# Optimization experiments

Hardware: AMD Instinct MI355X
Metric: run time of the kernel (lower is better)

Reference implementation:

```python
import jax, jax.numpy as jnp
import numpy as np

PAD = 0

def setup_inputs() -> dict:
    key = jax.random.key(0)
    ks = jax.random.split(key, 16)
    B, S, D, F = 64, 512, 768, 256
    VOCAB = 32000
    # variable-length tweets: length in [8, S], rest is padding (token id PAD=0)
    lengths = jax.random.randint(ks[0], (B,), 8, S + 1)
    tok = jax.random.randint(ks[1], (B, S), 1, VOCAB)
    x = jnp.where(jnp.arange(S)[None, :] < lengths[:, None], tok, PAD)
    h = jax.random.normal(ks[2], (B, S, D), dtype=jnp.float32)
    sc = 0.02
    w2 = jax.random.normal(ks[3], (F, D, 2), dtype=jnp.float32) * sc
    b2 = jax.random.normal(ks[4], (F,), dtype=jnp.float32) * sc
    w3 = jax.random.normal(ks[5], (F, D, 3), dtype=jnp.float32) * sc
    b3 = jax.random.normal(ks[6], (F,), dtype=jnp.float32) * sc
    w4 = jax.random.normal(ks[7], (F, D, 4), dtype=jnp.float32) * sc
    b4 = jax.random.normal(ks[8], (F,), dtype=jnp.float32) * sc
    w5 = jax.random.normal(ks[9], (F, D, 5), dtype=jnp.float32) * sc
    b5 = jax.random.normal(ks[10], (F,), dtype=jnp.float32) * sc
    fc_w = jax.random.normal(ks[11], (1, 4 * F), dtype=jnp.float32) * sc
    fc_b = jax.random.normal(ks[12], (1,), dtype=jnp.float32) * sc
    return {"x": x, "h": h, "w2": w2, "b2": b2, "w3": w3, "b3": b3,
            "w4": w4, "b4": b4, "w5": w5, "b5": b5, "fc_w": fc_w, "fc_b": fc_b}


def _branch(hc, L, w, b):
    # hc: [B, D, S] front-compacted hidden states; w: [F, D, k]
    k = w.shape[-1]
    out = jax.lax.conv_general_dilated(
        hc, w, window_strides=(1,), padding='VALID',
        dimension_numbers=('NCH', 'OIH', 'NCH')) + b[None, :, None]  # [B,F,S-k+1]
    T = out.shape[-1]
    # conv position t is valid iff t + k - 1 < L  <=>  t < L - k + 1
    valid = jnp.arange(T)[None, :] < (L - k + 1)[:, None]           # [B,T]
    neg = jnp.asarray(-jnp.inf, out.dtype)
    pooled = jnp.max(jnp.where(valid[:, None, :], out, neg), axis=-1)  # [B,F]
    return jax.nn.relu(pooled)


def reference(x, h, w2, b2, w3, b3, w4, b4, w5, b5, fc_w, fc_b):
    mask = x != PAD                                   # [B,S]
    L = mask.sum(axis=1)                              # [B]
    # stable compaction: move non-pad token hidden states to the front, order preserved
    order = jnp.argsort(jnp.logical_not(mask), axis=1, stable=True)   # [B,S]
    hc = jnp.take_along_axis(h, order[..., None], axis=1)             # [B,S,D]
    hc = hc.transpose(0, 2, 1)                                        # [B,D,S]
    feats = jnp.concatenate([
        _branch(hc, L, w2, b2),
        _branch(hc, L, w3, b3),
        _branch(hc, L, w4, b4),
        _branch(hc, L, w5, b5),
    ], axis=-1)                                       # [B, 4F]
    logits = feats @ fc_w.T + fc_b                    # [B,1]
    return jax.nn.sigmoid(logits).squeeze(-1)         # [B]
```

## Files before the change

kernel.cpp:

```cpp
#include <hip/hip_runtime.h>
#include <stdint.h>

#define Bn 64
#define Sn 512
#define SPn 520
#define Dn 768
#define JSTRIDE 196608
#define ABUF 16640
#define BSLOT 8192
#define QS_A 28.222222f
#define SAQ 0.035433072f

typedef int iv4 __attribute__((ext_vector_type(4)));

static __device__ __forceinline__ signed char q8(float f, float s) {
  float t = __builtin_rintf(f * s);
  t = fmaxf(-127.f, fminf(127.f, t));
  return (signed char)(int)t;
}

static __device__ __forceinline__ void gload16(const void* g, void* l) {
  __builtin_amdgcn_global_load_lds(
      (const __attribute__((address_space(1))) unsigned int*)g,
      (__attribute__((address_space(3))) unsigned int*)l, 16, 0, 0);
}

__global__ __launch_bounds__(256) void plan_kernel(
    const int* __restrict__ x, int* __restrict__ plan, int* __restrict__ rowmap,
    int* __restrict__ feats) {
  __shared__ int sL[64];
  __shared__ int sOff[65];
  int tid = threadIdx.x, lane = tid & 63, wv = tid >> 6;
  {
    int4 z = {0, 0, 0, 0};
    for (int i = tid * 4; i < 65536; i += 1024) *(int4*)(feats + i) = z;
  }
  for (int bb = wv; bb < 64; bb += 4) {
    int cnt = 0;
    for (int c = 0; c < 8; ++c) {
      unsigned long long m = __ballot(x[bb * Sn + c * 64 + lane] != 0);
      cnt += __popcll(m);
    }
    if (lane == 0) sL[bb] = cnt;
  }
  __syncthreads();
  if (tid < 64) {
    int L = sL[tid];
    int SL = (L + 15) & ~15;
    int pre = SL;
    #pragma unroll
    for (int off = 1; off < 64; off <<= 1) {
      int y = __shfl_up(pre, off);
      if (tid >= off) pre += y;
    }
    sOff[tid] = pre - SL;
    if (tid == 63) { sOff[64] = pre; plan[0] = (pre + 255) >> 8; }
  }
  __syncthreads();
  int M = sOff[64];
  for (int b = 0; b < 64; ++b) {
    int off = sOff[b], L = sL[b];
    int SL = (L + 15) & ~15;
    int enc = (b << 20) | (L << 10);
    for (int t = tid; t < SL; t += 256) rowmap[off + t] = enc | t;
  }
  for (int p = M + tid; p < M + 264; p += 256)
    rowmap[p] = 512;
}

__global__ __launch_bounds__(256) void stage_kernel(
    const int* __restrict__ x, const float* __restrict__ h,
    const float* __restrict__ w2, const float* __restrict__ w3,
    const float* __restrict__ w4, const float* __restrict__ w5,
    signed char* __restrict__ hcq, signed char* __restrict__ wq,
    float* __restrict__ fscale) {
  int tid = threadIdx.x, lane = tid & 63, wv = tid >> 6;
  if (blockIdx.x < 512) {
    int cidx = blockIdx.x;
    int b = cidx >> 3, rblk = cidx & 7;
    __shared__ unsigned long long masks[8];
    __shared__ short sidx[Sn];
    for (int c = wv; c < 8; c += 4) {
      unsigned long long m = __ballot(x[b * Sn + c * 64 + lane] != 0);
      if (lane == 0) masks[c] = m;
    }
    __syncthreads();
    int pref[9]; pref[0] = 0;
    #pragma unroll
    for (int c = 0; c < 8; ++c) pref[c + 1] = pref[c] + __popcll(masks[c]);
    int L = pref[8];
    for (int p = tid; p < Sn; p += 256) {
      int c = p >> 6, l = p & 63;
      unsigned long long m = masks[c];
      if ((m >> l) & 1ull)
        sidx[pref[c] + __popcll(m & ((1ull << l) - 1ull))] = (short)p;
    }
    __syncthreads();
    int r0 = rblk * 65;
    for (int r = r0 + wv; r < r0 + 65; r += 4) {
      if (r < L) {
        signed char* dst = hcq + ((size_t)b * SPn + r) * Dn;
        const float* src = h + ((size_t)b * Sn + sidx[r]) * Dn;
        #pragma unroll
        for (int c = 0; c < 3; ++c) {
          int d = c * 256 + lane * 4;
          float4 v = *(const float4*)(src + d);
          char4 o = { q8(v.x, QS_A), q8(v.y, QS_A), q8(v.z, QS_A), q8(v.w, QS_A) };
          *(char4*)(dst + d) = o;
        }
      }
    }
  } else {
    __shared__ float sf[3840];
    __shared__ float smax[4];
    int bb = blockIdx.x - 512;
    int br = bb >> 8, f = bb & 255, k = br + 2;
    const float* w = (br == 0) ? w2 : (br == 1) ? w3 : (br == 2) ? w4 : w5;
    int mBase = 256 * ((br * (br + 3)) >> 1);
    const float* src = w + (size_t)f * Dn * k;
    int n = Dn * k;
    float mx = 0.f;
    for (int e = tid; e < n; e += 256) {
      float v = src[e];
      sf[e] = v;
      mx = fmaxf(mx, fabsf(v));
    }
    #pragma unroll
    for (int off = 32; off; off >>= 1) mx = fmaxf(mx, __shfl_xor(mx, off));
    if (lane == 0) smax[wv] = mx;
    __syncthreads();
    float M = fmaxf(fmaxf(smax[0], smax[1]), fmaxf(smax[2], smax[3]));
    M = fmaxf(M, 1e-30f);
    if (tid == 0) fscale[br * 256 + f] = M / 127.f;
    float qs = 127.f / M;
    for (int j = 0; j < k; ++j) {
      signed char* dst = wq + (size_t)(mBase + j * 256 + f) * Dn;
      for (int d4 = tid * 4; d4 < Dn; d4 += 1024) {
        char4 o = { q8(sf[(d4 + 0) * k + j], qs), q8(sf[(d4 + 1) * k + j], qs),
                    q8(sf[(d4 + 2) * k + j], qs), q8(sf[(d4 + 3) * k + j], qs) };
        *(char4*)(dst + d4) = o;
      }
    }
  }
}

template<int KK>
static __device__ __forceinline__ void stageAll(
    int d0, char* sA, char* sB, const char* const (&gA)[2], const char* gAt,
    const char* gB0, int lane, int wvoff) {
  int buf = d0 & 1;
  char* bB = sB + buf * (KK * BSLOT);
  int doff = d0 * 64;
  #pragma unroll
  for (int tap = 0; tap < KK; ++tap)
    gload16(gB0 + tap * JSTRIDE + doff, bB + tap * BSLOT + wvoff);
  char* nA = sA + buf * ABUF;
  gload16(gA[0] + doff, nA + wvoff);
  gload16(gA[1] + doff, nA + 8192 + wvoff);
  if (lane < 16) gload16(gAt + doff, nA + 16384);
}

template<int KK>
static __device__ __forceinline__ void computeD0(
    int d0, const char* sA, const char* sB, int wr, int wc, int lrow, int lg,
    iv4 (&acc)[4][4]) {
  int buf = d0 & 1;
  const char* curA = sA + buf * ABUF;
  const char* bB = sB + buf * (KK * BSLOT);
  #pragma unroll
  for (int j = 0; j < KK; ++j) {
    const char* curB = bB + j * BSLOT;
    iv4 Af[4], Bf[4];
    #pragma unroll
    for (int n = 0; n < 4; ++n) {
      int row = wc * 64 + n * 16 + lrow;
      Bf[n] = *(const iv4*)(curB + row * 64 + ((lg ^ ((row >> 1) & 3)) << 4));
    }
    #pragma unroll
    for (int m = 0; m < 4; ++m) {
      int row = wr * 64 + m * 16 + lrow + j;
      Af[m] = *(const iv4*)(curA + row * 64 + ((lg ^ ((row >> 1) & 3)) << 4));
    }
    __builtin_amdgcn_s_setprio(1);
    #pragma unroll
    for (int n = 0; n < 4; ++n)
      #pragma unroll
      for (int m = 0; m < 4; ++m)
        acc[m][n] = __builtin_amdgcn_mfma_i32_16x16x64_i8(Af[m], Bf[n], acc[m][n], 0, 0, 0);
    __builtin_amdgcn_s_setprio(0);
  }
}

template<int KK>
static __device__ __forceinline__ void conv_loop(
    char* sA, char* sB, const char* const (&gA)[2], const char* gAt,
    const char* gB0, int lane, int wr, int wc, int lrow, int lg, int wvoff,
    iv4 (&acc)[4][4]) {
  stageAll<KK>(0, sA, sB, gA, gAt, gB0, lane, wvoff);
  __syncthreads();
  #pragma unroll 2
  for (int d0 = 0; d0 < 11; ++d0) {
    stageAll<KK>(d0 + 1, sA, sB, gA, gAt, gB0, lane, wvoff);
    computeD0<KK>(d0, sA, sB, wr, wc, lrow, lg, acc);
    __syncthreads();
  }
  computeD0<KK>(11, sA, sB, wr, wc, lrow, lg, acc);
}

__global__ __launch_bounds__(512) void conv_kernel(
    const signed char* __restrict__ hcq, const signed char* __restrict__ wq,
    const float* __restrict__ b2, const float* __restrict__ b3,
    const float* __restrict__ b4, const float* __restrict__ b5,
    const float* __restrict__ fscale,
    const int* __restrict__ plan, const int* __restrict__ rowmap,
    int* __restrict__ feats) {
  __shared__ char smem[2 * ABUF + 2 * 5 * BSLOT];
  char* sA = smem;
  char* sB = smem + 2 * ABUF;
  int idx = blockIdx.x;
  int xcd = idx & 7, s2 = idx >> 3;
  int sub = s2 & 7, tile = xcd + ((s2 >> 3) << 3);
  if (tile >= plan[0]) return;
  int br = 3 - (sub >> 1), ff = sub & 1, kk = br + 2;
  int mBase = 256 * ((br * (br + 3)) >> 1) + ff * 128;
  const float* bias = (br == 0) ? b2 : (br == 1) ? b3 : (br == 2) ? b4 : b5;
  int tid = threadIdx.x, lane = tid & 63, wv = tid >> 6;
  int wr = wv >> 1, wc = wv & 1;
  int lrow = lane & 15, lg = lane >> 4;
  int wvoff = wv * 1024;
  int P0 = tile << 8;

  const char* gA[2];
  #pragma unroll
  for (int p = 0; p < 2; ++p) {
    int c = p * 512 + tid;
    int row = c >> 2, sgp = c & 3;
    int rm = rowmap[P0 + row];
    int bb_ = rm >> 20, t = rm & 1023;
    int seg = sgp ^ ((row >> 1) & 3);
    gA[p] = (const char*)(hcq + ((size_t)(bb_ * SPn + t)) * Dn + seg * 16);
  }
  const char* gAt;
  {
    int l = lane & 15;
    int row = 256 + (l >> 2), sgp = l & 3;
    int rm = rowmap[P0 + row];
    int bb_ = rm >> 20, t = rm & 1023;
    int seg = sgp ^ ((row >> 1) & 3);
    gAt = (const char*)(hcq + ((size_t)(bb_ * SPn + t)) * Dn + seg * 16);
  }
  const char* gB0;
  {
    int row = tid >> 2, sgp = tid & 3;
    int seg = sgp ^ ((row >> 1) & 3);
    gB0 = (const char*)(wq + ((size_t)(mBase + row)) * Dn + seg * 16);
  }

  iv4 acc[4][4];
  #pragma unroll
  for (int m = 0; m < 4; ++m)
    #pragma unroll
    for (int n = 0; n < 4; ++n) acc[m][n] = (iv4)0;

  switch (br) {
    case 3: conv_loop<5>(sA, sB, gA, gAt, gB0, lane, wr, wc, lrow, lg, wvoff, acc); break;
    case 2: conv_loop<4>(sA, sB, gA, gAt, gB0, lane, wr, wc, lrow, lg, wvoff, acc); break;
    case 1: conv_loop<3>(sA, sB, gA, gAt, gB0, lane, wr, wc, lrow, lg, wvoff, acc); break;
    default: conv_loop<2>(sA, sB, gA, gAt, gB0, lane, wr, wc, lrow, lg, wvoff, acc); break;
  }

  int rmv[4];
  #pragma unroll
  for (int m = 0; m < 4; ++m) rmv[m] = rowmap[P0 + wr * 64 + m * 16];
  #pragma unroll
  for (int n = 0; n < 4; ++n) {
    int fg = ff * 128 + wc * 64 + n * 16 + lrow;
    float bv = bias[fg];
    float sfc = fscale[br * 256 + fg] * SAQ;
    #pragma unroll
    for (int m = 0; m < 4; ++m) {
      int bb_ = rmv[m] >> 20;
      int Lb = (rmv[m] >> 10) & 1023;
      int t0 = (rmv[m] & 1023) + lg * 4;
      int vlim = Lb - kk + 1;
      float pmax = 0.f;
      #pragma unroll
      for (int i = 0; i < 4; ++i) {
        float v = (float)acc[m][n][i] * sfc + bv;
        pmax = fmaxf(pmax, (t0 + i < vlim) ? fmaxf(v, 0.f) : 0.f);
      }
      pmax = fmaxf(pmax, __shfl_xor(pmax, 16));
      pmax = fmaxf(pmax, __shfl_xor(pmax, 32));
      if (lane < 16 && pmax > 0.f)
        atomicMax(feats + bb_ * 1024 + br * 256 + fg, __float_as_int(pmax));
    }
  }
}

__global__ __launch_bounds__(64) void fc_kernel(
    const int* __restrict__ feats, const float* __restrict__ fcw,
    const float* __restrict__ fcb, float* __restrict__ out) {
  int b = blockIdx.x, lane = threadIdx.x;
  float acc = 0.f;
  for (int i = lane; i < 1024; i += 64)
    acc += __int_as_float(feats[b * 1024 + i]) * fcw[i];
  #pragma unroll
  for (int off = 32; off; off >>= 1) acc += __shfl_xor(acc, off);
  if (lane == 0) out[b] = 1.f / (1.f + expf(-(acc + fcb[0])));
}

extern "C" void kernel_launch(void* const* d_in, const int* in_sizes, int n_in,
                              void* d_out, int out_size, void* d_ws, size_t ws_size,
                              hipStream_t stream) {
  const int*   x   = (const int*)d_in[0];
  const float* h   = (const float*)d_in[1];
  const float* w2  = (const float*)d_in[2];
  const float* b2  = (const float*)d_in[3];
  const float* w3  = (const float*)d_in[4];
  const float* b3  = (const float*)d_in[5];
  const float* w4  = (const float*)d_in[6];
  const float* b4  = (const float*)d_in[7];
  const float* w5  = (const float*)d_in[8];
  const float* b5  = (const float*)d_in[9];
  const float* fcw = (const float*)d_in[10];
  const float* fcb = (const float*)d_in[11];
  float* out = (float*)d_out;
  char* ws = (char*)d_ws;
  signed char* hcq = (signed char*)ws;
  signed char* wq  = (signed char*)(ws + 25559040);
  float* fscale = (float*)(ws + 28311552);
  int* feats  = (int*)(ws + 28315648);
  int* plan   = (int*)(ws + 28577792);
  int* rowmap = (int*)(ws + 28577808);

  plan_kernel<<<1, 256, 0, stream>>>(x, plan, rowmap, feats);
  stage_kernel<<<1536, 256, 0, stream>>>(x, h, w2, w3, w4, w5, hcq, wq, fscale);
  conv_kernel<<<1024, 512, 0, stream>>>(hcq, wq, b2, b3, b4, b5, fscale, plan, rowmap, feats);
  fc_kernel<<<64, 64, 0, stream>>>(feats, fcw, fcb, out);
}
```

Before: 110.0 us.

## Drop serial plan kernel, double-buffer MFMA fragments across taps

Removes the single-block plan kernel. Its feats zeroing becomes a memset, the length counts are written by stage_kernel, and the rowmap/plan construction moves to a parallel 64-block fill kernel. This targets the serialized one-block prologue that ran ahead of the big kernels. Separately, the conv inner loop now prefetches LDS fragments for the next tap into a second register set while the current tap's MFMAs issue, which overlaps LDS reads with matrix math at the cost of more registers.

Result: faster. 98.00 us (-11.0%).

```diff
diff --git a/kernel.cpp b/kernel.cpp
--- a/kernel.cpp
+++ b/kernel.cpp
@@ -25,47 +25,9 @@
       (__attribute__((address_space(3))) unsigned int*)l, 16, 0, 0);
 }
 
-__global__ __launch_bounds__(256) void plan_kernel(
-    const int* __restrict__ x, int* __restrict__ plan, int* __restrict__ rowmap,
-    int* __restrict__ feats) {
-  __shared__ int sL[64];
-  __shared__ int sOff[65];
-  int tid = threadIdx.x, lane = tid & 63, wv = tid >> 6;
-  {
-    int4 z = {0, 0, 0, 0};
-    for (int i = tid * 4; i < 65536; i += 1024) *(int4*)(feats + i) = z;
-  }
-  for (int bb = wv; bb < 64; bb += 4) {
-    int cnt = 0;
-    for (int c = 0; c < 8; ++c) {
-      unsigned long long m = __ballot(x[bb * Sn + c * 64 + lane] != 0);
-      cnt += __popcll(m);
-    }
-    if (lane == 0) sL[bb] = cnt;
-  }
-  __syncthreads();
-  if (tid < 64) {
-    int L = sL[tid];
-    int SL = (L + 15) & ~15;
-    int pre = SL;
-    #pragma unroll
-    for (int off = 1; off < 64; off <<= 1) {
-      int y = __shfl_up(pre, off);
-      if (tid >= off) pre += y;
-    }
-    sOff[tid] = pre - SL;
-    if (tid == 63) { sOff[64] = pre; plan[0] = (pre + 255) >> 8; }
-  }
-  __syncthreads();
-  int M = sOff[64];
-  for (int b = 0; b < 64; ++b) {
-    int off = sOff[b], L = sL[b];
-    int SL = (L + 15) & ~15;
-    int enc = (b << 20) | (L << 10);
-    for (int t = tid; t < SL; t += 256) rowmap[off + t] = enc | t;
-  }
-  for (int p = M + tid; p < M + 264; p += 256)
-    rowmap[p] = 512;
+template<int S, typename T, int N>
+static __device__ __forceinline__ T (&sel(T (&a)[N], T (&b)[N]))[N] {
+  if constexpr (S) return b; else return a;
 }
 
 __global__ __launch_bounds__(256) void stage_kernel(
@@ -73,7 +35,7 @@
     const float* __restrict__ w2, const float* __restrict__ w3,
     const float* __restrict__ w4, const float* __restrict__ w5,
     signed char* __restrict__ hcq, signed char* __restrict__ wq,
-    float* __restrict__ fscale) {
+    float* __restrict__ fscale, int* __restrict__ Lout) {
   int tid = threadIdx.x, lane = tid & 63, wv = tid >> 6;
   if (blockIdx.x < 512) {
     int cidx = blockIdx.x;
@@ -89,6 +51,7 @@
     #pragma unroll
     for (int c = 0; c < 8; ++c) pref[c + 1] = pref[c] + __popcll(masks[c]);
     int L = pref[8];
+    if (rblk == 0 && tid == 0) Lout[b] = L;
     for (int p = tid; p < Sn; p += 256) {
       int c = p >> 6, l = p & 63;
       unsigned long long m = masks[c];
@@ -144,6 +107,39 @@
   }
 }
 
+__global__ __launch_bounds__(256) void fill_kernel(
+    const int* __restrict__ Lbuf, int* __restrict__ plan,
+    int* __restrict__ rowmap) {
+  __shared__ int sOff[65];
+  __shared__ int sL[64];
+  int tid = threadIdx.x;
+  if (tid < 64) {
+    int L = Lbuf[tid];
+    int SL = (L + 15) & ~15;
+    int pre = SL;
+    #pragma unroll
+    for (int off = 1; off < 64; off <<= 1) {
+      int y = __shfl_up(pre, off);
+      if (tid >= off) pre += y;
+    }
+    sOff[tid] = pre - SL;
+    sL[tid] = L;
+    if (tid == 63) sOff[64] = pre;
+  }
+  __syncthreads();
+  int b = blockIdx.x;
+  int off = sOff[b], L = sL[b];
+  int SL = (L + 15) & ~15;
+  int enc = (b << 20) | (L << 10);
+  for (int t = tid; t < SL; t += 256) rowmap[off + t] = enc | t;
+  if (b == 0) {
+    int M = sOff[64];
+    if (tid == 0) plan[0] = (M + 255) >> 8;
+    for (int p = M + tid; p < M + 264; p += 256)
+      rowmap[p] = 512;
+  }
+}
+
 template<int KK>
 static __device__ __forceinline__ void stageAll(
     int d0, char* sA, char* sB, const char* const (&gA)[2], const char* gAt,
@@ -160,6 +156,41 @@
   if (lane < 16) gload16(gAt + doff, nA + 16384);
 }
 
+static __device__ __forceinline__ void readFrag(
+    int j, const char* curA, const char* bB, int wr, int wc, int lrow, int lg,
+    iv4 (&Af)[4], iv4 (&Bf)[4]) {
+  const char* curB = bB + j * BSLOT;
+  #pragma unroll
+  for (int n = 0; n < 4; ++n) {
+    int row = wc * 64 + n * 16 + lrow;
+    Bf[n] = *(const iv4*)(curB + row * 64 + ((lg ^ ((row >> 1) & 3)) << 4));
+  }
+  #pragma unroll
+  for (int m = 0; m < 4; ++m) {
+    int row = wr * 64 + m * 16 + lrow + j;
+    Af[m] = *(const iv4*)(curA + row * 64 + ((lg ^ ((row >> 1) & 3)) << 4));
+  }
+}
+
+template<int KK, int J>
+static __device__ __forceinline__ void jpass(
+    const char* curA, const char* bB, int wr, int wc, int lrow, int lg,
+    iv4 (&Af0)[4], iv4 (&Bf0)[4], iv4 (&Af1)[4], iv4 (&Bf1)[4],
+    iv4 (&acc)[4][4]) {
+  if constexpr (J + 1 < KK)
+    readFrag(J + 1, curA, bB, wr, wc, lrow, lg,
+             sel<(J + 1) & 1>(Af0, Af1), sel<(J + 1) & 1>(Bf0, Bf1));
+  iv4 (&Au)[4] = sel<J & 1>(Af0, Af1);
+  iv4 (&Bu)[4] = sel<J & 1>(Bf0, Bf1);
+  __builtin_amdgcn_s_setprio(1);
+  #pragma unroll
+  for (int n = 0; n < 4; ++n)
+    #pragma unroll
+    for (int m = 0; m < 4; ++m)
+      acc[m][n] = __builtin_amdgcn_mfma_i32_16x16x64_i8(Au[m], Bu[n], acc[m][n], 0, 0, 0);
+  __builtin_amdgcn_s_setprio(0);
+}
+
 template<int KK>
 static __device__ __forceinline__ void computeD0(
     int d0, const char* sA, const char* sB, int wr, int wc, int lrow, int lg,
@@ -167,28 +198,13 @@
   int buf = d0 & 1;
   const char* curA = sA + buf * ABUF;
   const char* bB = sB + buf * (KK * BSLOT);
-  #pragma unroll
-  for (int j = 0; j < KK; ++j) {
-    const char* curB = bB + j * BSLOT;
-    iv4 Af[4], Bf[4];
-    #pragma unroll
-    for (int n = 0; n < 4; ++n) {
-      int row = wc * 64 + n * 16 + lrow;
-      Bf[n] = *(const iv4*)(curB + row * 64 + ((lg ^ ((row >> 1) & 3)) << 4));
-    }
-    #pragma unroll
-    for (int m = 0; m < 4; ++m) {
-      int row = wr * 64 + m * 16 + lrow + j;
-      Af[m] = *(const iv4*)(curA + row * 64 + ((lg ^ ((row >> 1) & 3)) << 4));
-    }
-    __builtin_amdgcn_s_setprio(1);
-    #pragma unroll
-    for (int n = 0; n < 4; ++n)
-      #pragma unroll
-      for (int m = 0; m < 4; ++m)
-        acc[m][n] = __builtin_amdgcn_mfma_i32_16x16x64_i8(Af[m], Bf[n], acc[m][n], 0, 0, 0);
-    __builtin_amdgcn_s_setprio(0);
-  }
+  iv4 Af0[4], Bf0[4], Af1[4], Bf1[4];
+  readFrag(0, curA, bB, wr, wc, lrow, lg, Af0, Bf0);
+  jpass<KK, 0>(curA, bB, wr, wc, lrow, lg, Af0, Bf0, Af1, Bf1, acc);
+  if constexpr (KK > 1) jpass<KK, 1>(curA, bB, wr, wc, lrow, lg, Af0, Bf0, Af1, Bf1, acc);
+  if constexpr (KK > 2) jpass<KK, 2>(curA, bB, wr, wc, lrow, lg, Af0, Bf0, Af1, Bf1, acc);
+  if constexpr (KK > 3) jpass<KK, 3>(curA, bB, wr, wc, lrow, lg, Af0, Bf0, Af1, Bf1, acc);
+  if constexpr (KK > 4) jpass<KK, 4>(curA, bB, wr, wc, lrow, lg, Af0, Bf0, Af1, Bf1, acc);
 }
 
 template<int KK>
@@ -330,11 +346,13 @@
   signed char* wq  = (signed char*)(ws + 25559040);
   float* fscale = (float*)(ws + 28311552);
   int* feats  = (int*)(ws + 28315648);
-  int* plan   = (int*)(ws + 28577792);
-  int* rowmap = (int*)(ws + 28577808);
-
-  plan_kernel<<<1, 256, 0, stream>>>(x, plan, rowmap, feats);
-  stage_kernel<<<1536, 256, 0, stream>>>(x, h, w2, w3, w4, w5, hcq, wq, fscale);
+  int* Lbuf   = (int*)(ws + 28577792);
+  int* plan   = (int*)(ws + 28578048);
+  int* rowmap = (int*)(ws + 28578064);
+
+  hipMemsetAsync(feats, 0, 64 * 1024 * 4, stream);
+  stage_kernel<<<1536, 256, 0, stream>>>(x, h, w2, w3, w4, w5, hcq, wq, fscale, Lbuf);
+  fill_kernel<<<64, 256, 0, stream>>>(Lbuf, plan, rowmap);
   conv_kernel<<<1024, 512, 0, stream>>>(hcq, wq, b2, b3, b4, b5, fscale, plan, rowmap, feats);
   fc_kernel<<<64, 64, 0, stream>>>(feats, fcw, fcb, out);
 }
```
